# Kernel optimization log

Measured on AMD Instinct MI355X. Metric: run time of the kernel, lower is better.

The kernel has to match this reference:

```python
import jax, jax.numpy as jnp
import numpy as np

N_HEAD = 16
N_EMBD = 1024

def setup_inputs() -> dict:
    key = jax.random.key(0)
    ks = jax.random.split(key, 5)
    C = N_EMBD
    x = jax.random.normal(ks[0], (4, 2048, C), dtype=jnp.float32)
    s = 1.0 / np.sqrt(C)
    W_attn = jax.random.normal(ks[1], (C, 3 * C), dtype=jnp.float32) * s
    b_attn = jax.random.normal(ks[2], (3 * C,), dtype=jnp.float32) * 0.02
    W_proj = jax.random.normal(ks[3], (C, C), dtype=jnp.float32) * s
    b_proj = jax.random.normal(ks[4], (C,), dtype=jnp.float32) * 0.02
    return {"x": x, "W_attn": W_attn, "b_attn": b_attn, "W_proj": W_proj, "b_proj": b_proj}

def reference(x, W_attn, b_attn, W_proj, b_proj):
    B, T, C = x.shape
    H = C // N_HEAD
    qkv = x @ W_attn + b_attn  # [B,T,3C]
    q, k, v = jnp.split(qkv, 3, axis=2)
    # [B,T,C] -> [B,nh,T,H]
    q = q.reshape(B, T, N_HEAD, H).transpose(0, 2, 1, 3)
    k = k.reshape(B, T, N_HEAD, H).transpose(0, 2, 1, 3)
    v = v.reshape(B, T, N_HEAD, H).transpose(0, 2, 1, 3)
    att = jnp.einsum('bhqd,bhkd->bhqk', q, k) * (1.0 / np.sqrt(H).astype(np.float32))
    causal = jnp.tril(jnp.ones((T, T), dtype=bool))  # [T,T]
    att = jnp.where(causal, att, -jnp.inf)
    att = jax.nn.softmax(att, axis=-1)
    y = jnp.einsum('bhqk,bhkd->bhqd', att, v)
    y = y.transpose(0, 2, 1, 3).reshape(B, T, C)
    return y @ W_proj + b_proj
```

## Files before the change

kernel.cpp:

```cpp
#include <hip/hip_runtime.h>
#include <math.h>

#define T_LEN 2048
#define C_DIM 1024
#define C3    3072
#define NHEAD 16
#define HDIM  64

typedef __attribute__((ext_vector_type(8))) __bf16 bf16x8;
typedef __attribute__((ext_vector_type(8))) unsigned short u16x8;
typedef __attribute__((ext_vector_type(4))) float f32x4;
typedef unsigned short ushort_t;

#define QK_SCALE 0.180336878f

#if defined(__has_builtin)
#if __has_builtin(__builtin_amdgcn_exp2f)
#define FAST_EXP2(x) __builtin_amdgcn_exp2f(x)
#endif
#endif
#ifndef FAST_EXP2
#define FAST_EXP2(x) exp2f(x)
#endif

__device__ __forceinline__ ushort_t f2bf(float f) {
    unsigned int u = __float_as_uint(f);
    unsigned int r = (u + 0x7FFFu + ((u >> 16) & 1u)) >> 16;
    return (ushort_t)r;
}

#define GLL16(g, l) __builtin_amdgcn_global_load_lds( \
    (const __attribute__((address_space(1))) void*)(g), \
    (__attribute__((address_space(3))) void*)(l), 16, 0, 0)

__global__ __launch_bounds__(256) void prep_inputs(
    const float* __restrict__ x, ushort_t* __restrict__ xb,
    const float* __restrict__ W1, ushort_t* __restrict__ Wt1,
    const float* __restrict__ W2, ushort_t* __restrict__ Wt2)
{
    __shared__ float t[64][65];
    const int bx = blockIdx.x;
    if (bx < 8192) {
        const int i = bx * 256 + threadIdx.x;
        const float4 v = ((const float4*)x)[i];
        ushort4 o;
        o.x = f2bf(v.x); o.y = f2bf(v.y); o.z = f2bf(v.z); o.w = f2bf(v.w);
        ((ushort4*)xb)[i] = o;
        return;
    }
    const float* W; ushort_t* Wt; int N, n0, k0;
    if (bx < 8960) {
        const int tt = bx - 8192;
        W = W1; Wt = Wt1; N = C3;
        n0 = (tt % 48) * 64; k0 = (tt / 48) * 64;
    } else {
        const int tt = bx - 8960;
        W = W2; Wt = Wt2; N = C_DIM;
        n0 = (tt % 16) * 64; k0 = (tt / 16) * 64;
    }
    const int K = C_DIM;
    const int c = threadIdx.x & 63, r4 = threadIdx.x >> 6;
#pragma unroll
    for (int i = 0; i < 16; i++) {
        int r = i * 4 + r4;
        t[r][c] = W[(size_t)(k0 + r) * N + n0 + c];
    }
    __syncthreads();
#pragma unroll
    for (int i = 0; i < 16; i++) {
        int r = i * 4 + r4;
        Wt[(size_t)(n0 + r) * K + k0 + c] = f2bf(t[c][r]);
    }
}

template <bool OUT_BF16, bool QSCALE>
__global__ __launch_bounds__(256, 3) void gemm_bt_mfma(
    const ushort_t* __restrict__ A, const ushort_t* __restrict__ Bt,
    const float* __restrict__ bias, void* __restrict__ Cv,
    int M, int N, int K)
{
    __shared__ ushort_t Alds[128 * 64];
    __shared__ ushort_t Blds[128 * 64];

    const int tid = threadIdx.x;
    const int m0 = blockIdx.y * 128;
    const int n0 = blockIdx.x * 128;
    const int w = tid >> 6;
    const int ln = tid & 63;
    const int quad = ln >> 4;
    const int r16 = ln & 15;
    const int wr0 = (w & 1) * 64;
    const int wc0 = (w >> 1) * 64;

    f32x4 acc[4][4] = {};

    const int srow = tid >> 3;
    const int csrc8 = ((tid & 7) ^ (srow & 7)) * 8;
    const int sw = r16 & 7;

    for (int k0 = 0; k0 < K; k0 += 64) {
#pragma unroll
        for (int rr = 0; rr < 4; rr++) {
            const ushort_t* ga = A + (size_t)(m0 + rr * 32 + srow) * K + k0 + csrc8;
            GLL16(ga, Alds + rr * 2048 + tid * 8);
            const ushort_t* gb = Bt + (size_t)(n0 + rr * 32 + srow) * K + k0 + csrc8;
            GLL16(gb, Blds + rr * 2048 + tid * 8);
        }
        __syncthreads();

#pragma unroll
        for (int s = 0; s < 2; s++) {
            const int cpos = ((4 * s + quad) ^ sw) * 8;
            bf16x8 af[4], bfr[4];
#pragma unroll
            for (int i = 0; i < 4; i++)
                af[i] = *(const bf16x8*)(Alds + (wr0 + i * 16 + r16) * 64 + cpos);
#pragma unroll
            for (int j = 0; j < 4; j++)
                bfr[j] = *(const bf16x8*)(Blds + (wc0 + j * 16 + r16) * 64 + cpos);
#pragma unroll
            for (int i = 0; i < 4; i++)
#pragma unroll
                for (int j = 0; j < 4; j++)
                    acc[i][j] = __builtin_amdgcn_mfma_f32_16x16x32_bf16(
                        af[i], bfr[j], acc[i][j], 0, 0, 0);
        }
        __syncthreads();
    }

    const float scl = (QSCALE && n0 < C_DIM) ? QK_SCALE : 1.0f;

#pragma unroll
    for (int j = 0; j < 4; j++) {
        const int col = n0 + wc0 + j * 16 + r16;
        const float bv = bias[col];
#pragma unroll
        for (int i = 0; i < 4; i++) {
            const int rowb = m0 + wr0 + i * 16 + quad * 4;
#pragma unroll
            for (int r = 0; r < 4; r++) {
                const float v = (acc[i][j][r] + bv) * scl;
                if (OUT_BF16)
                    ((ushort_t*)Cv)[(size_t)(rowb + r) * N + col] = f2bf(v);
                else
                    ((float*)Cv)[(size_t)(rowb + r) * N + col] = v;
            }
        }
    }
}

__global__ __launch_bounds__(256) void transpose_v(
    const ushort_t* __restrict__ qkv, ushort_t* __restrict__ vtg)
{
    __shared__ ushort_t Ts[64][72];
    const int t0 = blockIdx.x * 64;
    const int bh = blockIdx.y;
    const int b = bh >> 4, h = bh & 15;
    const ushort_t* src = qkv + (size_t)b * T_LEN * C3 + 2 * C_DIM + h * HDIM;
    const int tid = threadIdx.x;
    {
        const int r = tid >> 2, cs = (tid & 3) * 16;
        *(u16x8*)(&Ts[r][cs])     = *(const u16x8*)(src + (size_t)(t0 + r) * C3 + cs);
        *(u16x8*)(&Ts[r][cs + 8]) = *(const u16x8*)(src + (size_t)(t0 + r) * C3 + cs + 8);
    }
    __syncthreads();
    {
        const int d = tid >> 2, ts0 = (tid & 3) * 16;
        ushort_t* dst = vtg + ((size_t)bh * HDIM + d) * T_LEN + t0 + ts0;
        u16x8 o0, o1;
#pragma unroll
        for (int j = 0; j < 8; j++) o0[j] = Ts[ts0 + j][d];
#pragma unroll
        for (int j = 0; j < 8; j++) o1[j] = Ts[ts0 + 8 + j][d];
        *(u16x8*)dst = o0;
        *(u16x8*)(dst + 8) = o1;
    }
}

#define QPITCH 72

__device__ __forceinline__ void softmax_store(
    f32x4 (&s)[4], float& lacc, ushort_t* __restrict__ QP,
    int prow, int quad)
{
#pragma unroll
    for (int mb = 0; mb < 4; mb++) {
        const float p0 = FAST_EXP2(s[mb][0]);
        const float p1 = FAST_EXP2(s[mb][1]);
        const float p2 = FAST_EXP2(s[mb][2]);
        const float p3 = FAST_EXP2(s[mb][3]);
        lacc += (p0 + p1) + (p2 + p3);
        uint2 pk;
        pk.x = __builtin_amdgcn_perm(__float_as_uint(p1), __float_as_uint(p0), 0x07060302u);
        pk.y = __builtin_amdgcn_perm(__float_as_uint(p3), __float_as_uint(p2), 0x07060302u);
        *(uint2*)(QP + prow * QPITCH + mb * 16 + quad * 4) = pk;
    }
}

__device__ __forceinline__ void mask_diag(f32x4 (&s)[4], int qloc, int quad)
{
#pragma unroll
    for (int mb = 0; mb < 4; mb++)
#pragma unroll
        for (int r = 0; r < 4; r++)
            if (mb * 16 + quad * 4 + r > qloc) s[mb][r] = -1e30f;
}

#define STAGE_KV(kt_, buf_) do {                                              \
    const int _k0 = (kt_) * 64;                                               \
    const int _bo = (buf_) * 4096;                                            \
    _Pragma("unroll")                                                         \
    for (int rr = 0; rr < 2; rr++) {                                          \
        const ushort_t* gk = basek + (size_t)(_k0 + rr * 32 + srow) * C3 + csrc8; \
        GLL16(gk, Ks + _bo + rr * 2048 + tid * 8);                            \
        const ushort_t* gv = vrow + (size_t)(rr * 32 + srow) * T_LEN + _k0 + csrc8; \
        GLL16(gv, Vs + _bo + rr * 2048 + tid * 8);                            \
    }                                                                         \
} while (0)

__global__ __launch_bounds__(256) void attn_flash_mfma5(
    const ushort_t* __restrict__ qkv, const ushort_t* __restrict__ vtg,
    ushort_t* __restrict__ y)
{
    __shared__ ushort_t QP[128 * QPITCH];
    __shared__ ushort_t Ks[2 * 64 * 64];
    __shared__ ushort_t Vs[2 * 64 * 64];

    const int i = blockIdx.x;
    const int bh = blockIdx.y;
    const int b = bh >> 4, h = bh & 15;
    const int qA0 = i * 64;
    const int qB0 = (31 - i) * 64;
    const int lastkt = 31 - i;

    const int tid = threadIdx.x;
    const int w = tid >> 6;
    const int ln = tid & 63;
    const int quad = ln >> 4;
    const int r16 = ln & 15;
    const int qloc = w * 16 + r16;
    const int prowA = qloc;
    const int prowB = 64 + qloc;

    const int srow = tid >> 3;
    const int csrc8 = ((tid & 7) ^ (srow & 7)) * 8;
    const int cpos0 = ((quad ^ (r16 & 7))) * 8;

    const ushort_t* baseq = qkv + (size_t)b * T_LEN * C3 + h * HDIM;
    const ushort_t* basek = baseq + C_DIM;
    const ushort_t* vrow = vtg + (size_t)bh * HDIM * T_LEN;

    STAGE_KV(0, 0);

#pragma unroll
    for (int it = 0; it < 4; it++) {
        int e = tid + it * 256;
        int r = e >> 3, c8 = (e & 7) * 8;
        int gq = (r < 64) ? (qA0 + r) : (qB0 + r - 64);
        *(u16x8*)(QP + r * QPITCH + c8) =
            *(const u16x8*)(baseq + (size_t)gq * C3 + c8);
    }
    __syncthreads();

    bf16x8 aqA[2], aqB[2];
#pragma unroll
    for (int s = 0; s < 2; s++) {
        aqA[s] = *(const bf16x8*)(QP + prowA * QPITCH + s * 32 + quad * 8);
        aqB[s] = *(const bf16x8*)(QP + prowB * QPITCH + s * 32 + quad * 8);
    }

    f32x4 oA[4] = {}, oB[4] = {};
    float lA = 0.0f, lB = 0.0f;

    for (int kt = 0; kt <= lastkt; kt++) {
        __syncthreads();

        if (kt < lastkt) STAGE_KV(kt + 1, (kt + 1) & 1);

        const int kb = (kt & 1) * 4096;

        if (kt <= i) {
            f32x4 sA[4] = {}, sB[4] = {};
#pragma unroll
            for (int s = 0; s < 2; s++)
#pragma unroll
                for (int mb = 0; mb < 4; mb++) {
                    const bf16x8 ak = *(const bf16x8*)(Ks + kb + (mb * 16 + r16) * 64 + (cpos0 ^ (s * 32)));
                    sA[mb] = __builtin_amdgcn_mfma_f32_16x16x32_bf16(ak, aqA[s], sA[mb], 0, 0, 0);
                    sB[mb] = __builtin_amdgcn_mfma_f32_16x16x32_bf16(ak, aqB[s], sB[mb], 0, 0, 0);
                }
            if (kt == i) mask_diag(sA, qloc, quad);
            softmax_store(sA, lA, QP, prowA, quad);
            softmax_store(sB, lB, QP, prowB, quad);
#pragma unroll
            for (int s = 0; s < 2; s++) {
                const bf16x8 bpA = *(const bf16x8*)(QP + prowA * QPITCH + s * 32 + quad * 8);
                const bf16x8 bpB = *(const bf16x8*)(QP + prowB * QPITCH + s * 32 + quad * 8);
#pragma unroll
                for (int mb = 0; mb < 4; mb++) {
                    const bf16x8 av = *(const bf16x8*)(Vs + kb + (mb * 16 + r16) * 64 + (cpos0 ^ (s * 32)));
                    oA[mb] = __builtin_amdgcn_mfma_f32_16x16x32_bf16(av, bpA, oA[mb], 0, 0, 0);
                    oB[mb] = __builtin_amdgcn_mfma_f32_16x16x32_bf16(av, bpB, oB[mb], 0, 0, 0);
                }
            }
        } else {
            f32x4 sB[4] = {};
#pragma unroll
            for (int s = 0; s < 2; s++)
#pragma unroll
                for (int mb = 0; mb < 4; mb++) {
                    const bf16x8 ak = *(const bf16x8*)(Ks + kb + (mb * 16 + r16) * 64 + (cpos0 ^ (s * 32)));
                    sB[mb] = __builtin_amdgcn_mfma_f32_16x16x32_bf16(ak, aqB[s], sB[mb], 0, 0, 0);
                }
            if (kt == lastkt) mask_diag(sB, qloc, quad);
            softmax_store(sB, lB, QP, prowB, quad);
#pragma unroll
            for (int s = 0; s < 2; s++) {
                const bf16x8 bpB = *(const bf16x8*)(QP + prowB * QPITCH + s * 32 + quad * 8);
#pragma unroll
                for (int mb = 0; mb < 4; mb++) {
                    const bf16x8 av = *(const bf16x8*)(Vs + kb + (mb * 16 + r16) * 64 + (cpos0 ^ (s * 32)));
                    oB[mb] = __builtin_amdgcn_mfma_f32_16x16x32_bf16(av, bpB, oB[mb], 0, 0, 0);
                }
            }
        }
    }

    lA += __shfl_xor(lA, 16); lA += __shfl_xor(lA, 32);
    lB += __shfl_xor(lB, 16); lB += __shfl_xor(lB, 32);
    {
        const float invA = 1.0f / lA;
        ushort_t* yp = y + ((size_t)(b * T_LEN + qA0 + qloc)) * C_DIM + h * HDIM;
#pragma unroll
        for (int mb = 0; mb < 4; mb++) {
            ushort4 o;
            o.x = f2bf(oA[mb][0] * invA);
            o.y = f2bf(oA[mb][1] * invA);
            o.z = f2bf(oA[mb][2] * invA);
            o.w = f2bf(oA[mb][3] * invA);
            *(ushort4*)(yp + mb * 16 + quad * 4) = o;
        }
    }
    {
        const float invB = 1.0f / lB;
        ushort_t* yp = y + ((size_t)(b * T_LEN + qB0 + qloc)) * C_DIM + h * HDIM;
#pragma unroll
        for (int mb = 0; mb < 4; mb++) {
            ushort4 o;
            o.x = f2bf(oB[mb][0] * invB);
            o.y = f2bf(oB[mb][1] * invB);
            o.z = f2bf(oB[mb][2] * invB);
            o.w = f2bf(oB[mb][3] * invB);
            *(ushort4*)(yp + mb * 16 + quad * 4) = o;
        }
    }
}

extern "C" void kernel_launch(void* const* d_in, const int* in_sizes, int n_in,
                              void* d_out, int out_size, void* d_ws, size_t ws_size,
                              hipStream_t stream)
{
    const float* x      = (const float*)d_in[0];
    const float* W_attn = (const float*)d_in[1];
    const float* b_attn = (const float*)d_in[2];
    const float* W_proj = (const float*)d_in[3];
    const float* b_proj = (const float*)d_in[4];
    float* out = (float*)d_out;

    const int M = 4 * T_LEN;
    char* ws = (char*)d_ws;
    ushort_t* qkv = (ushort_t*)ws;
    ushort_t* xb  = (ushort_t*)(ws + 50331648);
    ushort_t* Wt1 = (ushort_t*)(ws + 67108864);
    ushort_t* yb  = (ushort_t*)(ws + 73400320);
    ushort_t* Wt2 = (ushort_t*)(ws + 90177536);
    ushort_t* vtg = (ushort_t*)(ws + 92274688);

    prep_inputs<<<9216, 256, 0, stream>>>(x, xb, W_attn, Wt1, W_proj, Wt2);

    gemm_bt_mfma<true, true><<<dim3(C3 / 128, M / 128), 256, 0, stream>>>(
        xb, Wt1, b_attn, qkv, M, C3, C_DIM);

    transpose_v<<<dim3(T_LEN / 64, 4 * NHEAD), 256, 0, stream>>>(qkv, vtg);

    attn_flash_mfma5<<<dim3(16, 4 * NHEAD), 256, 0, stream>>>(qkv, vtg, yb);

    gemm_bt_mfma<false, false><<<dim3(C_DIM / 128, M / 128), 256, 0, stream>>>(
        yb, Wt2, b_proj, out, M, C_DIM, C_DIM);
}
```

Baseline: 280.3 us.

## Single-buffer V staged in-iteration with mid-loop barrier; XOR-swizzle Q/P LDS tile

V tiles drop from double buffering to a single buffer. They are now loaded at the start of each iteration and overlapped with the QK^T MFMAs and softmax, with a partial vmcnt wait plus a barrier placed before the PV stage. K stays double-buffered and prefetched one tile ahead. The Q/P shared tile drops its padded pitch in favour of an XOR swizzle, which saves LDS and is meant to avoid bank conflicts. The aim is lower LDS use, which may help occupancy, and hiding V load latency behind the score compute. The cost is an extra barrier per iteration and reliance on hand-written waitcnt counts being correct.

```diff
diff --git a/kernel.cpp b/kernel.cpp
--- a/kernel.cpp
+++ b/kernel.cpp
@@ -177,11 +177,10 @@
     }
 }
 
-#define QPITCH 72
 
 __device__ __forceinline__ void softmax_store(
     f32x4 (&s)[4], float& lacc, ushort_t* __restrict__ QP,
-    int prow, int quad)
+    int prow, int quad, int sw)
 {
 #pragma unroll
     for (int mb = 0; mb < 4; mb++) {
@@ -193,7 +192,7 @@
         uint2 pk;
         pk.x = __builtin_amdgcn_perm(__float_as_uint(p1), __float_as_uint(p0), 0x07060302u);
         pk.y = __builtin_amdgcn_perm(__float_as_uint(p3), __float_as_uint(p2), 0x07060302u);
-        *(uint2*)(QP + prow * QPITCH + mb * 16 + quad * 4) = pk;
+        *(uint2*)(QP + prow * 64 + ((2 * mb + (quad >> 1)) ^ sw) * 8 + (quad & 1) * 4) = pk;
     }
 }
 
@@ -206,15 +205,22 @@
             if (mb * 16 + quad * 4 + r > qloc) s[mb][r] = -1e30f;
 }
 
-#define STAGE_KV(kt_, buf_) do {                                              \
+#define STAGE_V(kt_) do {                                                     \
+    const int _k0 = (kt_) * 64;                                               \
+    _Pragma("unroll")                                                         \
+    for (int rr = 0; rr < 2; rr++) {                                          \
+        const ushort_t* gv = vrow + (size_t)(rr * 32 + srow) * T_LEN + _k0 + csrc8; \
+        GLL16(gv, Vs + rr * 2048 + tid * 8);                                  \
+    }                                                                         \
+} while (0)
+
+#define STAGE_K(kt_, buf_) do {                                               \
     const int _k0 = (kt_) * 64;                                               \
     const int _bo = (buf_) * 4096;                                            \
     _Pragma("unroll")                                                         \
     for (int rr = 0; rr < 2; rr++) {                                          \
         const ushort_t* gk = basek + (size_t)(_k0 + rr * 32 + srow) * C3 + csrc8; \
         GLL16(gk, Ks + _bo + rr * 2048 + tid * 8);                            \
-        const ushort_t* gv = vrow + (size_t)(rr * 32 + srow) * T_LEN + _k0 + csrc8; \
-        GLL16(gv, Vs + _bo + rr * 2048 + tid * 8);                            \
     }                                                                         \
 } while (0)
 
@@ -222,9 +228,9 @@
     const ushort_t* __restrict__ qkv, const ushort_t* __restrict__ vtg,
     ushort_t* __restrict__ y)
 {
-    __shared__ ushort_t QP[128 * QPITCH];
+    __shared__ ushort_t QP[128 * 64];
     __shared__ ushort_t Ks[2 * 64 * 64];
-    __shared__ ushort_t Vs[2 * 64 * 64];
+    __shared__ ushort_t Vs[64 * 64];
 
     const int i = blockIdx.x;
     const int bh = blockIdx.y;
@@ -241,41 +247,43 @@
     const int qloc = w * 16 + r16;
     const int prowA = qloc;
     const int prowB = 64 + qloc;
+    const int sw = r16 & 7;
 
     const int srow = tid >> 3;
     const int csrc8 = ((tid & 7) ^ (srow & 7)) * 8;
-    const int cpos0 = ((quad ^ (r16 & 7))) * 8;
+    const int cpos0 = (quad ^ sw) * 8;
 
     const ushort_t* baseq = qkv + (size_t)b * T_LEN * C3 + h * HDIM;
     const ushort_t* basek = baseq + C_DIM;
     const ushort_t* vrow = vtg + (size_t)bh * HDIM * T_LEN;
 
-    STAGE_KV(0, 0);
+    STAGE_K(0, 0);
 
 #pragma unroll
     for (int it = 0; it < 4; it++) {
         int e = tid + it * 256;
-        int r = e >> 3, c8 = (e & 7) * 8;
+        int r = e >> 3, c = e & 7;
         int gq = (r < 64) ? (qA0 + r) : (qB0 + r - 64);
-        *(u16x8*)(QP + r * QPITCH + c8) =
-            *(const u16x8*)(baseq + (size_t)gq * C3 + c8);
+        *(u16x8*)(QP + r * 64 + ((c ^ (r & 7)) * 8)) =
+            *(const u16x8*)(baseq + (size_t)gq * C3 + c * 8);
     }
     __syncthreads();
 
     bf16x8 aqA[2], aqB[2];
 #pragma unroll
     for (int s = 0; s < 2; s++) {
-        aqA[s] = *(const bf16x8*)(QP + prowA * QPITCH + s * 32 + quad * 8);
-        aqB[s] = *(const bf16x8*)(QP + prowB * QPITCH + s * 32 + quad * 8);
+        aqA[s] = *(const bf16x8*)(QP + prowA * 64 + (cpos0 ^ (s * 32)));
+        aqB[s] = *(const bf16x8*)(QP + prowB * 64 + (cpos0 ^ (s * 32)));
     }
 
     f32x4 oA[4] = {}, oB[4] = {};
     float lA = 0.0f, lB = 0.0f;
 
     for (int kt = 0; kt <= lastkt; kt++) {
-        __syncthreads();
-
-        if (kt < lastkt) STAGE_KV(kt + 1, (kt + 1) & 1);
+        if (kt) __syncthreads();
+
+        STAGE_V(kt);
+        if (kt < lastkt) STAGE_K(kt + 1, (kt + 1) & 1);
 
         const int kb = (kt & 1) * 4096;
 
@@ -290,15 +298,21 @@
                     sB[mb] = __builtin_amdgcn_mfma_f32_16x16x32_bf16(ak, aqB[s], sB[mb], 0, 0, 0);
                 }
             if (kt == i) mask_diag(sA, qloc, quad);
-            softmax_store(sA, lA, QP, prowA, quad);
-            softmax_store(sB, lB, QP, prowB, quad);
+            softmax_store(sA, lA, QP, prowA, quad, sw);
+            softmax_store(sB, lB, QP, prowB, quad, sw);
+
+            if (kt < lastkt) asm volatile("s_waitcnt vmcnt(2)" ::: "memory");
+            else             asm volatile("s_waitcnt vmcnt(0)" ::: "memory");
+            __builtin_amdgcn_s_barrier();
+            __builtin_amdgcn_sched_barrier(0);
+
 #pragma unroll
             for (int s = 0; s < 2; s++) {
-                const bf16x8 bpA = *(const bf16x8*)(QP + prowA * QPITCH + s * 32 + quad * 8);
-                const bf16x8 bpB = *(const bf16x8*)(QP + prowB * QPITCH + s * 32 + quad * 8);
+                const bf16x8 bpA = *(const bf16x8*)(QP + prowA * 64 + (cpos0 ^ (s * 32)));
+                const bf16x8 bpB = *(const bf16x8*)(QP + prowB * 64 + (cpos0 ^ (s * 32)));
 #pragma unroll
                 for (int mb = 0; mb < 4; mb++) {
-                    const bf16x8 av = *(const bf16x8*)(Vs + kb + (mb * 16 + r16) * 64 + (cpos0 ^ (s * 32)));
+                    const bf16x8 av = *(const bf16x8*)(Vs + (mb * 16 + r16) * 64 + (cpos0 ^ (s * 32)));
                     oA[mb] = __builtin_amdgcn_mfma_f32_16x16x32_bf16(av, bpA, oA[mb], 0, 0, 0);
                     oB[mb] = __builtin_amdgcn_mfma_f32_16x16x32_bf16(av, bpB, oB[mb], 0, 0, 0);
                 }
@@ -313,13 +327,19 @@
                     sB[mb] = __builtin_amdgcn_mfma_f32_16x16x32_bf16(ak, aqB[s], sB[mb], 0, 0, 0);
                 }
             if (kt == lastkt) mask_diag(sB, qloc, quad);
-            softmax_store(sB, lB, QP, prowB, quad);
+            softmax_store(sB, lB, QP, prowB, quad, sw);
+
+            if (kt < lastkt) asm volatile("s_waitcnt vmcnt(2)" ::: "memory");
+            else             asm volatile("s_waitcnt vmcnt(0)" ::: "memory");
+            __builtin_amdgcn_s_barrier();
+            __builtin_amdgcn_sched_barrier(0);
+
 #pragma unroll
             for (int s = 0; s < 2; s++) {
-                const bf16x8 bpB = *(const bf16x8*)(QP + prowB * QPITCH + s * 32 + quad * 8);
+                const bf16x8 bpB = *(const bf16x8*)(QP + prowB * 64 + (cpos0 ^ (s * 32)));
 #pragma unroll
                 for (int mb = 0; mb < 4; mb++) {
-                    const bf16x8 av = *(const bf16x8*)(Vs + kb + (mb * 16 + r16) * 64 + (cpos0 ^ (s * 32)));
+                    const bf16x8 av = *(const bf16x8*)(Vs + (mb * 16 + r16) * 64 + (cpos0 ^ (s * 32)));
                     oB[mb] = __builtin_amdgcn_mfma_f32_16x16x32_bf16(av, bpB, oB[mb], 0, 0, 0);
                 }
             }
```

Measured after the change: 273.7 us. 2.4% less time.

## Exchange softmax probabilities via permlane swaps instead of LDS round-trip

Applied to the files above, without the earlier changes.

Replaces the LDS write/read of the bf16 probability tile between the QK and PV MFMAs with in-register cross-lane exchange using v_permlane32_swap and v_permlane16_swap, turning the S accumulator layout into the B-operand layout. Q fragments are now loaded directly from global memory rather than staged through shared memory, which removes the QP buffer and cuts LDS usage. Launch bounds now request 4 blocks per CU. This depends on the permlane mapping producing the correct operand order, and may raise register pressure.

```diff
diff --git a/kernel.cpp b/kernel.cpp
--- a/kernel.cpp
+++ b/kernel.cpp
@@ -10,6 +10,7 @@
 typedef __attribute__((ext_vector_type(8))) __bf16 bf16x8;
 typedef __attribute__((ext_vector_type(8))) unsigned short u16x8;
 typedef __attribute__((ext_vector_type(4))) float f32x4;
+typedef __attribute__((ext_vector_type(2))) unsigned int u32x2;
 typedef unsigned short ushort_t;
 
 #define QK_SCALE 0.180336878f
@@ -17,6 +18,9 @@
 #if defined(__has_builtin)
 #if __has_builtin(__builtin_amdgcn_exp2f)
 #define FAST_EXP2(x) __builtin_amdgcn_exp2f(x)
+#endif
+#if __has_builtin(__builtin_amdgcn_permlane32_swap) && __has_builtin(__builtin_amdgcn_permlane16_swap)
+#define HAVE_PERMLANE_SWAP 1
 #endif
 #endif
 #ifndef FAST_EXP2
@@ -177,12 +181,20 @@
     }
 }
 
-#define QPITCH 72
-
-__device__ __forceinline__ void softmax_store(
-    f32x4 (&s)[4], float& lacc, ushort_t* __restrict__ QP,
-    int prow, int quad)
-{
+
+__device__ __forceinline__ void mask_diag(f32x4 (&s)[4], int qloc, int quad)
+{
+#pragma unroll
+    for (int mb = 0; mb < 4; mb++)
+#pragma unroll
+        for (int r = 0; r < 4; r++)
+            if (mb * 16 + quad * 4 + r > qloc) s[mb][r] = -1e30f;
+}
+
+__device__ __forceinline__ void softmax_exchange(
+    f32x4 (&s)[4], float& lacc, bf16x8 (&bp)[2])
+{
+    unsigned int pk[4][2];
 #pragma unroll
     for (int mb = 0; mb < 4; mb++) {
         const float p0 = FAST_EXP2(s[mb][0]);
@@ -190,39 +202,59 @@
         const float p2 = FAST_EXP2(s[mb][2]);
         const float p3 = FAST_EXP2(s[mb][3]);
         lacc += (p0 + p1) + (p2 + p3);
-        uint2 pk;
-        pk.x = __builtin_amdgcn_perm(__float_as_uint(p1), __float_as_uint(p0), 0x07060302u);
-        pk.y = __builtin_amdgcn_perm(__float_as_uint(p3), __float_as_uint(p2), 0x07060302u);
-        *(uint2*)(QP + prow * QPITCH + mb * 16 + quad * 4) = pk;
-    }
-}
-
-__device__ __forceinline__ void mask_diag(f32x4 (&s)[4], int qloc, int quad)
-{
-#pragma unroll
-    for (int mb = 0; mb < 4; mb++)
-#pragma unroll
-        for (int r = 0; r < 4; r++)
-            if (mb * 16 + quad * 4 + r > qloc) s[mb][r] = -1e30f;
-}
-
-#define STAGE_KV(kt_, buf_) do {                                              \
+        pk[mb][0] = __builtin_amdgcn_perm(__float_as_uint(p1), __float_as_uint(p0), 0x07060302u);
+        pk[mb][1] = __builtin_amdgcn_perm(__float_as_uint(p3), __float_as_uint(p2), 0x07060302u);
+    }
+#pragma unroll
+    for (int s2 = 0; s2 < 2; s2++) {
+        uint4 t;
+#pragma unroll
+        for (int u = 0; u < 2; u++) {
+            unsigned int A = pk[2 * s2][u], B = pk[2 * s2 + 1][u];
+            unsigned int out1, out2;
+#ifdef HAVE_PERMLANE_SWAP
+            u32x2 r1 = __builtin_amdgcn_permlane32_swap(A, B, false, false);
+            u32x2 r2 = __builtin_amdgcn_permlane16_swap(r1.x, r1.y, false, false);
+            out1 = r2.x; out2 = r2.y;
+#else
+            asm volatile("s_nop 1\n\t"
+                         "v_permlane32_swap_b32 %0, %1\n\t"
+                         "s_nop 1\n\t"
+                         "v_permlane16_swap_b32 %0, %1"
+                         : "+v"(A), "+v"(B));
+            out1 = A; out2 = B;
+#endif
+            if (u == 0) { t.x = out1; t.z = out2; }
+            else        { t.y = out1; t.w = out2; }
+        }
+        bp[s2] = *(bf16x8*)&t;
+    }
+}
+
+#define STAGE_K(kt_, buf_) do {                                               \
     const int _k0 = (kt_) * 64;                                               \
     const int _bo = (buf_) * 4096;                                            \
     _Pragma("unroll")                                                         \
     for (int rr = 0; rr < 2; rr++) {                                          \
         const ushort_t* gk = basek + (size_t)(_k0 + rr * 32 + srow) * C3 + csrc8; \
         GLL16(gk, Ks + _bo + rr * 2048 + tid * 8);                            \
+    }                                                                         \
+} while (0)
+
+#define STAGE_V(kt_, buf_) do {                                               \
+    const int _k0 = (kt_) * 64;                                               \
+    const int _bo = (buf_) * 4096;                                            \
+    _Pragma("unroll")                                                         \
+    for (int rr = 0; rr < 2; rr++) {                                          \
         const ushort_t* gv = vrow + (size_t)(rr * 32 + srow) * T_LEN + _k0 + csrc8; \
         GLL16(gv, Vs + _bo + rr * 2048 + tid * 8);                            \
     }                                                                         \
 } while (0)
 
-__global__ __launch_bounds__(256) void attn_flash_mfma5(
+__global__ __launch_bounds__(256, 4) void attn_flash_mfma5(
     const ushort_t* __restrict__ qkv, const ushort_t* __restrict__ vtg,
     ushort_t* __restrict__ y)
 {
-    __shared__ ushort_t QP[128 * QPITCH];
     __shared__ ushort_t Ks[2 * 64 * 64];
     __shared__ ushort_t Vs[2 * 64 * 64];
 
@@ -239,34 +271,24 @@
     const int quad = ln >> 4;
     const int r16 = ln & 15;
     const int qloc = w * 16 + r16;
-    const int prowA = qloc;
-    const int prowB = 64 + qloc;
+    const int sw = r16 & 7;
 
     const int srow = tid >> 3;
     const int csrc8 = ((tid & 7) ^ (srow & 7)) * 8;
-    const int cpos0 = ((quad ^ (r16 & 7))) * 8;
+    const int cpos0 = (quad ^ sw) * 8;
 
     const ushort_t* baseq = qkv + (size_t)b * T_LEN * C3 + h * HDIM;
     const ushort_t* basek = baseq + C_DIM;
     const ushort_t* vrow = vtg + (size_t)bh * HDIM * T_LEN;
 
-    STAGE_KV(0, 0);
-
-#pragma unroll
-    for (int it = 0; it < 4; it++) {
-        int e = tid + it * 256;
-        int r = e >> 3, c8 = (e & 7) * 8;
-        int gq = (r < 64) ? (qA0 + r) : (qB0 + r - 64);
-        *(u16x8*)(QP + r * QPITCH + c8) =
-            *(const u16x8*)(baseq + (size_t)gq * C3 + c8);
-    }
-    __syncthreads();
+    STAGE_K(0, 0);
+    STAGE_V(0, 0);
 
     bf16x8 aqA[2], aqB[2];
 #pragma unroll
     for (int s = 0; s < 2; s++) {
-        aqA[s] = *(const bf16x8*)(QP + prowA * QPITCH + s * 32 + quad * 8);
-        aqB[s] = *(const bf16x8*)(QP + prowB * QPITCH + s * 32 + quad * 8);
+        aqA[s] = *(const bf16x8*)(baseq + (size_t)(qA0 + qloc) * C3 + s * 32 + quad * 8);
+        aqB[s] = *(const bf16x8*)(baseq + (size_t)(qB0 + qloc) * C3 + s * 32 + quad * 8);
     }
 
     f32x4 oA[4] = {}, oB[4] = {};
@@ -275,7 +297,10 @@
     for (int kt = 0; kt <= lastkt; kt++) {
         __syncthreads();
 
-        if (kt < lastkt) STAGE_KV(kt + 1, (kt + 1) & 1);
+        if (kt < lastkt) {
+            STAGE_K(kt + 1, (kt + 1) & 1);
+            STAGE_V(kt + 1, (kt + 1) & 1);
+        }
 
         const int kb = (kt & 1) * 4096;
 
@@ -290,19 +315,17 @@
                     sB[mb] = __builtin_amdgcn_mfma_f32_16x16x32_bf16(ak, aqB[s], sB[mb], 0, 0, 0);
                 }
             if (kt == i) mask_diag(sA, qloc, quad);
-            softmax_store(sA, lA, QP, prowA, quad);
-            softmax_store(sB, lB, QP, prowB, quad);
-#pragma unroll
-            for (int s = 0; s < 2; s++) {
-                const bf16x8 bpA = *(const bf16x8*)(QP + prowA * QPITCH + s * 32 + quad * 8);
-                const bf16x8 bpB = *(const bf16x8*)(QP + prowB * QPITCH + s * 32 + quad * 8);
+            bf16x8 bpA[2], bpB[2];
+            softmax_exchange(sA, lA, bpA);
+            softmax_exchange(sB, lB, bpB);
+#pragma unroll
+            for (int s = 0; s < 2; s++)
 #pragma unroll
                 for (int mb = 0; mb < 4; mb++) {
                     const bf16x8 av = *(const bf16x8*)(Vs + kb + (mb * 16 + r16) * 64 + (cpos0 ^ (s * 32)));
-                    oA[mb] = __builtin_amdgcn_mfma_f32_16x16x32_bf16(av, bpA, oA[mb], 0, 0, 0);
-                    oB[mb] = __builtin_amdgcn_mfma_f32_16x16x32_bf16(av, bpB, oB[mb], 0, 0, 0);
+                    oA[mb] = __builtin_amdgcn_mfma_f32_16x16x32_bf16(av, bpA[s], oA[mb], 0, 0, 0);
+                    oB[mb] = __builtin_amdgcn_mfma_f32_16x16x32_bf16(av, bpB[s], oB[mb], 0, 0, 0);
                 }
-            }
         } else {
             f32x4 sB[4] = {};
 #pragma unroll
@@ -313,16 +336,15 @@
                     sB[mb] = __builtin_amdgcn_mfma_f32_16x16x32_bf16(ak, aqB[s], sB[mb], 0, 0, 0);
                 }
             if (kt == lastkt) mask_diag(sB, qloc, quad);
-            softmax_store(sB, lB, QP, prowB, quad);
-#pragma unroll
-            for (int s = 0; s < 2; s++) {
-                const bf16x8 bpB = *(const bf16x8*)(QP + prowB * QPITCH + s * 32 + quad * 8);
+            bf16x8 bpB[2];
+            softmax_exchange(sB, lB, bpB);
+#pragma unroll
+            for (int s = 0; s < 2; s++)
 #pragma unroll
                 for (int mb = 0; mb < 4; mb++) {
                     const bf16x8 av = *(const bf16x8*)(Vs + kb + (mb * 16 + r16) * 64 + (cpos0 ^ (s * 32)));
-                    oB[mb] = __builtin_amdgcn_mfma_f32_16x16x32_bf16(av, bpB, oB[mb], 0, 0, 0);
+                    oB[mb] = __builtin_amdgcn_mfma_f32_16x16x32_bf16(av, bpB[s], oB[mb], 0, 0, 0);
                 }
-            }
         }
     }
 
```

Result: faster. 263.9 us (-5.8%).
